# Kernel tuning notes

Measured on AMD Instinct MI355X. Metric: run time of the kernel, lower is better.

## Reference

```python
import jax, jax.numpy as jnp
import numpy as np

N, CIN, OUT, G, K = 16, 128, 128, 8, 56
GP = OUT // G  # group_planes = 16
EPS = 1e-5


def _bn(x, gamma, beta, mean, var, caxis):
    # inference-mode batchnorm over channel axis `caxis`
    shape = [1] * x.ndim
    shape[caxis] = x.shape[caxis]
    g = gamma.reshape(shape)
    b = beta.reshape(shape)
    m = mean.reshape(shape)
    v = var.reshape(shape)
    return (x - m) * (g * jax.lax.rsqrt(v + EPS)) + b


def setup_inputs() -> dict:
    key = jax.random.key(0)
    ks = jax.random.split(key, 16)
    d = {}
    d['x'] = jax.random.normal(ks[0], (N, CIN, K, K), jnp.float32)
    d['w_qkv'] = jax.random.normal(ks[1], (2 * OUT, CIN), jnp.float32) * np.float32(np.sqrt(1.0 / CIN))
    d['relative'] = jax.random.normal(ks[2], (2 * GP, 2 * K - 1), jnp.float32) * np.float32(np.sqrt(1.0 / GP))

    def bn_params(k, c):
        k1, k2, k3, k4 = jax.random.split(k, 4)
        gamma = 1.0 + 0.1 * jax.random.normal(k1, (c,), jnp.float32)
        beta = 0.05 * jax.random.normal(k2, (c,), jnp.float32)
        mean = 0.05 * jax.random.normal(k3, (c,), jnp.float32)
        var = 1.0 + 0.1 * jax.random.uniform(k4, (c,), jnp.float32)
        return gamma, beta, mean, var

    d['qkv_gamma'], d['qkv_beta'], d['qkv_mean'], d['qkv_var'] = bn_params(ks[3], 2 * OUT)
    d['sim_gamma'], d['sim_beta'], d['sim_mean'], d['sim_var'] = bn_params(ks[4], 3 * G)
    d['out_gamma'], d['out_beta'], d['out_mean'], d['out_var'] = bn_params(ks[5], 2 * OUT)
    return d


def reference(x, w_qkv, relative,
              qkv_gamma, qkv_beta, qkv_mean, qkv_var,
              sim_gamma, sim_beta, sim_mean, sim_var,
              out_gamma, out_beta, out_mean, out_var):
    n, c, h, w = x.shape  # width=False: attend along H
    xb = jnp.transpose(x, (0, 3, 1, 2)).reshape(n * w, c, h)  # [B, C, H], B = N*W

    # 1x1 conv qkv + BN1d
    qkv = jnp.einsum('oc,bch->boh', w_qkv, xb)  # [B, 2*OUT, H]
    qkv = _bn(qkv, qkv_gamma, qkv_beta, qkv_mean, qkv_var, 1)
    qkv = qkv.reshape(n * w, G, 2 * GP, h)
    hp = GP // 2
    q, k, v = qkv[:, :, :hp], qkv[:, :, hp:2 * hp], qkv[:, :, 2 * hp:]

    # relative position embeddings
    qi = jnp.arange(K)[None, :]
    ki = jnp.arange(K)[:, None]
    flat_idx = (ki - qi + K - 1).reshape(-1)  # [K*K]
    all_emb = relative[:, flat_idx].reshape(2 * GP, K, K)
    q_emb, k_emb, v_emb = all_emb[:hp], all_emb[hp:2 * hp], all_emb[2 * hp:]

    qr = jnp.einsum('bgci,cij->bgij', q, q_emb)
    kr = jnp.einsum('bgci,cij->bgij', k, k_emb).transpose(0, 1, 3, 2)
    qk = jnp.einsum('bgci,bgcj->bgij', q, k)

    stacked = jnp.concatenate([qk, qr, kr], axis=1)  # [B, 3G, H, H]
    stacked = _bn(stacked, sim_gamma, sim_beta, sim_mean, sim_var, 1)
    sim = stacked.reshape(n * w, 3, G, h, h).sum(axis=1)  # [B, G, H, H]
    sim = jax.nn.softmax(sim, axis=3)

    sv = jnp.einsum('bgij,bgcj->bgci', sim, v)      # [B, G, GP, H]
    sve = jnp.einsum('bgij,cij->bgci', sim, v_emb)  # [B, G, GP, H]
    # torch cat(dim=-1) then view(B, 2*OUT, H) == stack on a new axis before H
    stacked_out = jnp.concatenate([sv[:, :, :, None, :], sve[:, :, :, None, :]], axis=3)
    stacked_out = stacked_out.reshape(n * w, 2 * OUT, h)
    out = _bn(stacked_out, out_gamma, out_beta, out_mean, out_var, 1)
    out = out.reshape(n, w, OUT, 2, h).sum(axis=3)  # [N, W, OUT, H]
    out = jnp.transpose(out, (0, 2, 3, 1))  # [N, OUT, H, W]
    return out
```

## Files before the change

### kernel.cpp

```cpp
#include <hip/hip_runtime.h>
#include <hip/hip_bf16.h>
#include <cstddef>

#define EPSV 1e-5f

typedef __attribute__((ext_vector_type(8))) short bf16x8;
typedef __attribute__((ext_vector_type(4))) float f32x4;
typedef __attribute__((ext_vector_type(4))) short short4v;
typedef __attribute__((ext_vector_type(4))) int int4v;

__device__ __forceinline__ float b2f(short s) {
  union { unsigned u; float f; } x;
  x.u = ((unsigned)(unsigned short)s) << 16;
  return x.f;
}
__device__ __forceinline__ short f2b(float f) {
  union { __hip_bfloat16 h; short s; } x;
  x.h = __float2bfloat16(f);
  return x.s;
}

#define PF_W    3300000
#define PF_RQ   3316384
#define PF_RK   3327136
#define PF_RV   3337888
#define PF_QSC  3346592
#define PF_QSH  3346848
#define PF_OSC  3347104
#define PF_OSH  3347360
#define PF_SH3  3347616

__global__ __launch_bounds__(256) void k_prep(
    const float* __restrict__ wq, const float* __restrict__ rel,
    const float* __restrict__ qg, const float* __restrict__ qb,
    const float* __restrict__ qm, const float* __restrict__ qv,
    const float* __restrict__ sg, const float* __restrict__ sb,
    const float* __restrict__ sm, const float* __restrict__ svar,
    const float* __restrict__ og, const float* __restrict__ ob,
    const float* __restrict__ om, const float* __restrict__ ov,
    float* __restrict__ prep) {
  const int g = blockIdx.x;
  const int tid = threadIdx.x;
  const float scA = sg[g] * rsqrtf(svar[g] + EPSV);
  const float scB = sg[8 + g] * rsqrtf(svar[8 + g] + EPSV);
  const float scC = sg[16 + g] * rsqrtf(svar[16 + g] + EPSV);
  const float rCA = scC / scA;

  short* wb = (short*)(prep + PF_W) + g * 4096;
  for (int t = tid; t < 1024; t += 256) {
    int o = t >> 5, c0 = (t & 31) * 4;
    float4 wv = *(const float4*)&wq[g * 4096 + o * 128 + c0];
    short4v s4 = {f2b(wv.x), f2b(wv.y), f2b(wv.z), f2b(wv.w)};
    *(short4v*)&wb[o * 128 + c0] = s4;
  }
  float* rq = prep + PF_RQ + g * 1344;
  float* rk = prep + PF_RK + g * 1344;
  for (int t = tid; t < 1344; t += 256) {
    int d = t / 12, c = t - d * 12;
    rq[t] = (c < 8 && d < 111) ? rel[c * 111 + d] * scB : 0.f;
    rk[t] = (c < 8 && d < 111) ? rel[(8 + c) * 111 + d] * rCA : 0.f;
  }
  short* rv = (short*)(prep + PF_RV) + g * 2176;
  for (int t = tid; t < 2176; t += 256) {
    int c = t / 136, d = t - c * 136;
    rv[t] = (d < 111) ? f2b(rel[(16 + c) * 111 + d]) : (short)0;
  }
  if (tid < 32) {
    int ch = g * 32 + tid;
    float sc = qg[ch] * rsqrtf(qv[ch] + EPSV);
    float sh = qb[ch] - qm[ch] * sc;
    if (tid >= 8 && tid < 16) { sc *= scA; sh *= scA; }
    prep[PF_QSC + ch] = sc;
    prep[PF_QSH + ch] = sh;
    float so = og[ch] * rsqrtf(ov[ch] + EPSV);
    prep[PF_OSC + ch] = so;
    prep[PF_OSH + ch] = ob[ch] - om[ch] * so;
  }
  if (tid == 0) {
    float shA = sb[g] - sm[g] * scA;
    float shB = sb[8 + g] - sm[8 + g] * scB;
    float shC = sb[16 + g] - sm[16 + g] * scC;
    prep[PF_SH3 + g] = shA + shB + shC;
  }
}

__global__ __launch_bounds__(256) void k_transpose_in(const float* __restrict__ x,
                                                      unsigned* __restrict__ xbT) {
  const int nh = blockIdx.x;
  const int n = nh / 56, h = nh - n * 56;
  __shared__ short t2[128 * 57];
  const float* src = x + (size_t)n * 401408 + h * 56;
  for (int t = threadIdx.x; t < 1792; t += 256) {
    int c = t / 14, w4 = (t - c * 14) * 4;
    float4 v = *(const float4*)&src[c * 3136 + w4];
    t2[c * 57 + w4 + 0] = f2b(v.x);
    t2[c * 57 + w4 + 1] = f2b(v.y);
    t2[c * 57 + w4 + 2] = f2b(v.z);
    t2[c * 57 + w4 + 3] = f2b(v.w);
  }
  __syncthreads();
  for (int t = threadIdx.x; t < 3584; t += 256) {
    int w = t >> 6, cp = t & 63;
    unsigned lo = (unsigned short)t2[(2 * cp) * 57 + w];
    unsigned hi = (unsigned short)t2[(2 * cp + 1) * 57 + w];
    xbT[(((size_t)(n * 56 + w) * 56 + h) << 6) + cp] = lo | (hi << 16);
  }
}

__global__ __launch_bounds__(256) void k_transpose_out(const float* __restrict__ tmp,
                                                       float* __restrict__ out) {
  int nc = blockIdx.x;
  int n = nc >> 7, c = nc & 127;
  __shared__ float t[56][57];
  for (int idx = threadIdx.x; idx < 3136; idx += 256) {
    int w = idx / 56, h = idx - w * 56;
    t[h][w] = tmp[((size_t)(n * 56 + w) * 128 + c) * 56 + h];
  }
  __syncthreads();
  float* dst = out + (size_t)nc * 3136;
  for (int idx = threadIdx.x; idx < 3136; idx += 256)
    dst[idx] = t[idx / 56][idx % 56];
}

#define O_XST    0
#define O_SHFT   0
#define O_WS     7680
#define O_SIMA   7680
#define O_QKT    12288
#define O_SVL    12288
#define O_RQTF   14528
#define O_RKTF   17216
#define O_RELV   19904
#define O_VBH    22080
#define O_VBL    23232
#define SB_SH    24384

__global__ __launch_bounds__(512) void k_fused(
    const short* __restrict__ xbT, const float* __restrict__ prep,
    float* __restrict__ tmp) {
  const int tid = threadIdx.x;
  const int g = blockIdx.x / 896;
  const int b = blockIdx.x - g * 896;

  __shared__ __align__(16) short SB[SB_SH];
  __shared__ float s_qsc[32], s_qsh[32], s_osc[32], s_osh[32], s_sh3;

  const int lane = tid & 63;
  const int w = tid >> 6;
  const int m = lane & 15;
  const int qd = lane >> 4;
  const int it = w >> 1;
  const int half = w & 1;
  const int grp = tid >> 4;
  const int l16 = tid & 15;

  {
    int4v z = {0, 0, 0, 0};
    int4v* zp = (int4v*)(SB + O_VBH);
    for (int i = tid; i < 288; i += 512) zp[i] = z;

    const short* xsrc = xbT + (size_t)b * 7168;
    for (int t = tid; t < 896; t += 512) {
      int h = t >> 4, ck = (t & 15) * 8;
      *(bf16x8*)&SB[O_XST + h * 136 + ck] = *(const bf16x8*)&xsrc[h * 128 + ck];
    }
    const short* wsrc = (const short*)(prep + PF_W) + g * 4096;
    for (int t = tid; t < 512; t += 512) {
      int o = t >> 4, ck = (t & 15) * 8;
      *(bf16x8*)&SB[O_WS + o * 136 + ck] = *(const bf16x8*)&wsrc[o * 128 + ck];
    }
    const f32x4* rqp = (const f32x4*)(prep + PF_RQ + g * 1344);
    const f32x4* rkp = (const f32x4*)(prep + PF_RK + g * 1344);
    f32x4* rqd = (f32x4*)(SB + O_RQTF);
    f32x4* rkd = (f32x4*)(SB + O_RKTF);
    for (int t = tid; t < 672; t += 512) {
      if (t < 336) rqd[t] = rqp[t];
      else         rkd[t - 336] = rkp[t - 336];
    }
    const int4v* rvp = (const int4v*)((const short*)(prep + PF_RV) + g * 2176);
    int4v* rvd = (int4v*)(SB + O_RELV);
    for (int t = tid; t < 272; t += 512) rvd[t] = rvp[t];
    if (tid < 32) {
      s_qsc[tid] = prep[PF_QSC + g * 32 + tid];
      s_qsh[tid] = prep[PF_QSH + g * 32 + tid];
      s_osc[tid] = prep[PF_OSC + g * 32 + tid];
      s_osh[tid] = prep[PF_OSH + g * 32 + tid];
    }
    if (tid == 0) s_sh3 = prep[PF_SH3 + g];
  }
  __syncthreads();

  {
    const int o = half * 16 + m;
    const int h = it * 16 + m;
    f32x4 acc = {0.f, 0.f, 0.f, 0.f};
#pragma unroll
    for (int ks = 0; ks < 4; ++ks) {
      bf16x8 av = *(bf16x8*)&SB[O_WS + o * 136 + qd * 8 + ks * 32];
      bf16x8 bv = *(bf16x8*)&SB[O_XST + h * 136 + qd * 8 + ks * 32];
      acc = __builtin_amdgcn_mfma_f32_16x16x32_bf16(av, bv, acc, 0, 0, 0);
    }
    if (h < 56) {
      float* qkTf = (float*)(SB + O_QKT);
      if (half == 0) {
        float4 o4;
        o4.x = fmaf(acc[0], s_qsc[qd * 4 + 0], s_qsh[qd * 4 + 0]);
        o4.y = fmaf(acc[1], s_qsc[qd * 4 + 1], s_qsh[qd * 4 + 1]);
        o4.z = fmaf(acc[2], s_qsc[qd * 4 + 2], s_qsh[qd * 4 + 2]);
        o4.w = fmaf(acc[3], s_qsc[qd * 4 + 3], s_qsh[qd * 4 + 3]);
        *(float4*)&qkTf[h * 20 + qd * 4] = o4;
      } else {
#pragma unroll
        for (int r = 0; r < 4; ++r) {
          int cv = qd * 4 + r;
          float val = fmaf(acc[r], s_qsc[16 + cv], s_qsh[16 + cv]);
          short vh = f2b(val);
          short vl = f2b(val - b2f(vh));
          SB[O_VBH + cv * 72 + h] = vh;
          SB[O_VBL + cv * 72 + h] = vl;
        }
      }
    }
  }
  __syncthreads();

  {
    const float* qkTf = (const float*)(SB + O_QKT);
    const float* rqf = (const float*)(SB + O_RQTF);
    const float* rkf = (const float*)(SB + O_RKTF);
    const float sh3 = s_sh3;
    const int4v z = {0, 0, 0, 0};

    float4 kv0[4], kv1[4];
#pragma unroll
    for (int jt = 0; jt < 4; ++jt) {
      int j = jt * 16 + l16;
      int jj = (j < 56) ? j : 0;
      kv0[jt] = *(const float4*)&qkTf[jj * 20 + 8];
      kv1[jt] = *(const float4*)&qkTf[jj * 20 + 12];
    }

#pragma unroll
    for (int pass = 0; pass < 2; ++pass) {
      int i = pass * 32 + grp;
      if (i < 64 && l16 < 15) *(int4v*)&SB[O_SHFT + i * 120 + l16 * 8] = z;
      if (i < 56) {
        float4 qa = *(const float4*)&qkTf[i * 20 + 0];
        float4 qb4 = *(const float4*)&qkTf[i * 20 + 4];
        float L[4];
#pragma unroll
        for (int jt = 0; jt < 4; ++jt) {
          int j = jt * 16 + l16;
          if (j < 56) {
            const float4 rq0 = *(const float4*)&rqf[(i - j + 55) * 12];
            const float4 rq1 = *(const float4*)&rqf[(i - j + 55) * 12 + 4];
            const float4 rk0 = *(const float4*)&rkf[(j - i + 55) * 12];
            const float4 rk1 = *(const float4*)&rkf[(j - i + 55) * 12 + 4];
            const float4 k0 = kv0[jt], k1 = kv1[jt];
            float acc = sh3;
            acc = fmaf(qa.x, k0.x, acc);  acc = fmaf(qa.y, k0.y, acc);
            acc = fmaf(qa.z, k0.z, acc);  acc = fmaf(qa.w, k0.w, acc);
            acc = fmaf(qb4.x, k1.x, acc); acc = fmaf(qb4.y, k1.y, acc);
            acc = fmaf(qb4.z, k1.z, acc); acc = fmaf(qb4.w, k1.w, acc);
            acc = fmaf(qa.x, rq0.x, acc);  acc = fmaf(qa.y, rq0.y, acc);
            acc = fmaf(qa.z, rq0.z, acc);  acc = fmaf(qa.w, rq0.w, acc);
            acc = fmaf(qb4.x, rq1.x, acc); acc = fmaf(qb4.y, rq1.y, acc);
            acc = fmaf(qb4.z, rq1.z, acc); acc = fmaf(qb4.w, rq1.w, acc);
            acc = fmaf(k0.x, rk0.x, acc);  acc = fmaf(k0.y, rk0.y, acc);
            acc = fmaf(k0.z, rk0.z, acc);  acc = fmaf(k0.w, rk0.w, acc);
            acc = fmaf(k1.x, rk1.x, acc);  acc = fmaf(k1.y, rk1.y, acc);
            acc = fmaf(k1.w, rk1.w, acc);  acc = fmaf(k1.z, rk1.z, acc);
            L[jt] = acc;
          } else {
            L[jt] = -3.0e38f;
          }
        }
        float mx = fmaxf(fmaxf(L[0], L[1]), fmaxf(L[2], L[3]));
#pragma unroll
        for (int off = 1; off < 16; off <<= 1) mx = fmaxf(mx, __shfl_xor(mx, off));
        float sum = 0.f, ex[4];
#pragma unroll
        for (int jt = 0; jt < 4; ++jt) {
          ex[jt] = __expf(L[jt] - mx);
          sum += ex[jt];
        }
#pragma unroll
        for (int off = 1; off < 16; off <<= 1) sum += __shfl_xor(sum, off);
        float inv = 1.0f / sum;
#pragma unroll
        for (int jt = 0; jt < 4; ++jt) {
          int j = jt * 16 + l16;
          if (j < 56) {
            short pv = f2b(ex[jt] * inv);
            SB[O_SIMA + i * 72 + j] = pv;
            SB[O_SHFT + i * 120 + (i - j + 55)] = pv;
          } else {
            SB[O_SIMA + i * 72 + j] = 0;
          }
        }
      }
    }
  }
  __syncthreads();

  f32x4 sveacc = {0.f, 0.f, 0.f, 0.f};
  {
    if (half == 0) {
      bf16x8 pa0 = *(bf16x8*)&SB[O_SIMA + (it * 16 + m) * 72 + qd * 8];
      bf16x8 pa1 = *(bf16x8*)&SB[O_SIMA + (it * 16 + m) * 72 + qd * 8 + 32];
      f32x4 acc = {0.f, 0.f, 0.f, 0.f};
      bf16x8 bv;
      bv = *(bf16x8*)&SB[O_VBH + m * 72 + qd * 8];
      acc = __builtin_amdgcn_mfma_f32_16x16x32_bf16(pa0, bv, acc, 0, 0, 0);
      bv = *(bf16x8*)&SB[O_VBH + m * 72 + qd * 8 + 32];
      acc = __builtin_amdgcn_mfma_f32_16x16x32_bf16(pa1, bv, acc, 0, 0, 0);
      bv = *(bf16x8*)&SB[O_VBL + m * 72 + qd * 8];
      acc = __builtin_amdgcn_mfma_f32_16x16x32_bf16(pa0, bv, acc, 0, 0, 0);
      bv = *(bf16x8*)&SB[O_VBL + m * 72 + qd * 8 + 32];
      acc = __builtin_amdgcn_mfma_f32_16x16x32_bf16(pa1, bv, acc, 0, 0, 0);
      float* svLf = (float*)(SB + O_SVL);
#pragma unroll
      for (int r = 0; r < 4; ++r) {
        int i2 = it * 16 + qd * 4 + r;
        if (i2 < 56) svLf[m * 60 + i2] = acc[r];
      }
    } else {
#pragma unroll
      for (int ks = 0; ks < 4; ++ks) {
        bf16x8 av = *(bf16x8*)&SB[O_RELV + m * 136 + qd * 8 + ks * 32];
        bf16x8 bv = *(bf16x8*)&SB[O_SHFT + (it * 16 + m) * 120 + qd * 8 + ks * 32];
        sveacc = __builtin_amdgcn_mfma_f32_16x16x32_bf16(av, bv, sveacc, 0, 0, 0);
      }
    }
  }
  __syncthreads();

  if (half == 1) {
    const int i2 = it * 16 + m;
    if (i2 < 56) {
      const float* svLf = (const float*)(SB + O_SVL);
#pragma unroll
      for (int r = 0; r < 4; ++r) {
        int c = qd * 4 + r;
        float svv = svLf[c * 60 + i2];
        float o = fmaf(svv, s_osc[2 * c], s_osh[2 * c]) +
                  fmaf(sveacc[r], s_osc[2 * c + 1], s_osh[2 * c + 1]);
        tmp[((size_t)b * 128 + g * 16 + c) * 56 + i2] = o;
      }
    }
  }
}

extern "C" void kernel_launch(void* const* d_in, const int* in_sizes, int n_in,
                              void* d_out, int out_size, void* d_ws, size_t ws_size,
                              hipStream_t stream) {
  const float* x   = (const float*)d_in[0];
  const float* wq  = (const float*)d_in[1];
  const float* rel = (const float*)d_in[2];
  const float* qg = (const float*)d_in[3];
  const float* qb = (const float*)d_in[4];
  const float* qm = (const float*)d_in[5];
  const float* qv = (const float*)d_in[6];
  const float* sg = (const float*)d_in[7];
  const float* sb = (const float*)d_in[8];
  const float* sm = (const float*)d_in[9];
  const float* sv = (const float*)d_in[10];
  const float* og = (const float*)d_in[11];
  const float* ob = (const float*)d_in[12];
  const float* om = (const float*)d_in[13];
  const float* ov = (const float*)d_in[14];
  float* out = (float*)d_out;

  float* tmp = (float*)d_ws;

  k_prep<<<8, 256, 0, stream>>>(wq, rel, qg, qb, qm, qv,
                                sg, sb, sm, sv, og, ob, om, ov, out);
  k_transpose_in<<<896, 256, 0, stream>>>(x, (unsigned*)out);
  k_fused<<<7168, 512, 0, stream>>>((const short*)out, out, tmp);
  k_transpose_out<<<2048, 256, 0, stream>>>(tmp, out);
}
```

Baseline: 115.0 us.

## Merge prep and input transpose kernels, store intermediate in bf16, add MFMA priority

```diff
diff --git a/kernel.cpp b/kernel.cpp
--- a/kernel.cpp
+++ b/kernel.cpp
@@ -30,8 +30,9 @@
 #define PF_OSH  3347360
 #define PF_SH3  3347616
 
-__global__ __launch_bounds__(256) void k_prep(
-    const float* __restrict__ wq, const float* __restrict__ rel,
+__global__ __launch_bounds__(256) void k_prep_tin(
+    const float* __restrict__ x, const float* __restrict__ wq,
+    const float* __restrict__ rel,
     const float* __restrict__ qg, const float* __restrict__ qb,
     const float* __restrict__ qm, const float* __restrict__ qv,
     const float* __restrict__ sg, const float* __restrict__ sb,
@@ -39,82 +40,83 @@
     const float* __restrict__ og, const float* __restrict__ ob,
     const float* __restrict__ om, const float* __restrict__ ov,
     float* __restrict__ prep) {
-  const int g = blockIdx.x;
+  __shared__ short t2[128 * 57];
   const int tid = threadIdx.x;
-  const float scA = sg[g] * rsqrtf(svar[g] + EPSV);
-  const float scB = sg[8 + g] * rsqrtf(svar[8 + g] + EPSV);
-  const float scC = sg[16 + g] * rsqrtf(svar[16 + g] + EPSV);
-  const float rCA = scC / scA;
-
-  short* wb = (short*)(prep + PF_W) + g * 4096;
-  for (int t = tid; t < 1024; t += 256) {
-    int o = t >> 5, c0 = (t & 31) * 4;
-    float4 wv = *(const float4*)&wq[g * 4096 + o * 128 + c0];
-    short4v s4 = {f2b(wv.x), f2b(wv.y), f2b(wv.z), f2b(wv.w)};
-    *(short4v*)&wb[o * 128 + c0] = s4;
-  }
-  float* rq = prep + PF_RQ + g * 1344;
-  float* rk = prep + PF_RK + g * 1344;
-  for (int t = tid; t < 1344; t += 256) {
-    int d = t / 12, c = t - d * 12;
-    rq[t] = (c < 8 && d < 111) ? rel[c * 111 + d] * scB : 0.f;
-    rk[t] = (c < 8 && d < 111) ? rel[(8 + c) * 111 + d] * rCA : 0.f;
-  }
-  short* rv = (short*)(prep + PF_RV) + g * 2176;
-  for (int t = tid; t < 2176; t += 256) {
-    int c = t / 136, d = t - c * 136;
-    rv[t] = (d < 111) ? f2b(rel[(16 + c) * 111 + d]) : (short)0;
-  }
-  if (tid < 32) {
-    int ch = g * 32 + tid;
-    float sc = qg[ch] * rsqrtf(qv[ch] + EPSV);
-    float sh = qb[ch] - qm[ch] * sc;
-    if (tid >= 8 && tid < 16) { sc *= scA; sh *= scA; }
-    prep[PF_QSC + ch] = sc;
-    prep[PF_QSH + ch] = sh;
-    float so = og[ch] * rsqrtf(ov[ch] + EPSV);
-    prep[PF_OSC + ch] = so;
-    prep[PF_OSH + ch] = ob[ch] - om[ch] * so;
-  }
-  if (tid == 0) {
-    float shA = sb[g] - sm[g] * scA;
-    float shB = sb[8 + g] - sm[8 + g] * scB;
-    float shC = sb[16 + g] - sm[16 + g] * scC;
-    prep[PF_SH3 + g] = shA + shB + shC;
-  }
-}
-
-__global__ __launch_bounds__(256) void k_transpose_in(const float* __restrict__ x,
-                                                      unsigned* __restrict__ xbT) {
-  const int nh = blockIdx.x;
-  const int n = nh / 56, h = nh - n * 56;
-  __shared__ short t2[128 * 57];
-  const float* src = x + (size_t)n * 401408 + h * 56;
-  for (int t = threadIdx.x; t < 1792; t += 256) {
-    int c = t / 14, w4 = (t - c * 14) * 4;
-    float4 v = *(const float4*)&src[c * 3136 + w4];
-    t2[c * 57 + w4 + 0] = f2b(v.x);
-    t2[c * 57 + w4 + 1] = f2b(v.y);
-    t2[c * 57 + w4 + 2] = f2b(v.z);
-    t2[c * 57 + w4 + 3] = f2b(v.w);
-  }
-  __syncthreads();
-  for (int t = threadIdx.x; t < 3584; t += 256) {
-    int w = t >> 6, cp = t & 63;
-    unsigned lo = (unsigned short)t2[(2 * cp) * 57 + w];
-    unsigned hi = (unsigned short)t2[(2 * cp + 1) * 57 + w];
-    xbT[(((size_t)(n * 56 + w) * 56 + h) << 6) + cp] = lo | (hi << 16);
-  }
-}
-
-__global__ __launch_bounds__(256) void k_transpose_out(const float* __restrict__ tmp,
+
+  if (blockIdx.x < 8) {
+    const int g = blockIdx.x;
+    const float scA = sg[g] * rsqrtf(svar[g] + EPSV);
+    const float scB = sg[8 + g] * rsqrtf(svar[8 + g] + EPSV);
+    const float scC = sg[16 + g] * rsqrtf(svar[16 + g] + EPSV);
+    const float rCA = scC / scA;
+
+    short* wb = (short*)(prep + PF_W) + g * 4096;
+    for (int t = tid; t < 1024; t += 256) {
+      int o = t >> 5, c0 = (t & 31) * 4;
+      float4 wv = *(const float4*)&wq[g * 4096 + o * 128 + c0];
+      short4v s4 = {f2b(wv.x), f2b(wv.y), f2b(wv.z), f2b(wv.w)};
+      *(short4v*)&wb[o * 128 + c0] = s4;
+    }
+    float* rq = prep + PF_RQ + g * 1344;
+    float* rk = prep + PF_RK + g * 1344;
+    for (int t = tid; t < 1344; t += 256) {
+      int d = t / 12, c = t - d * 12;
+      rq[t] = (c < 8 && d < 111) ? rel[c * 111 + d] * scB : 0.f;
+      rk[t] = (c < 8 && d < 111) ? rel[(8 + c) * 111 + d] * rCA : 0.f;
+    }
+    short* rv = (short*)(prep + PF_RV) + g * 2176;
+    for (int t = tid; t < 2176; t += 256) {
+      int c = t / 136, d = t - c * 136;
+      rv[t] = (d < 111) ? f2b(rel[(16 + c) * 111 + d]) : (short)0;
+    }
+    if (tid < 32) {
+      int ch = g * 32 + tid;
+      float sc = qg[ch] * rsqrtf(qv[ch] + EPSV);
+      float sh = qb[ch] - qm[ch] * sc;
+      if (tid >= 8 && tid < 16) { sc *= scA; sh *= scA; }
+      prep[PF_QSC + ch] = sc;
+      prep[PF_QSH + ch] = sh;
+      float so = og[ch] * rsqrtf(ov[ch] + EPSV);
+      prep[PF_OSC + ch] = so;
+      prep[PF_OSH + ch] = ob[ch] - om[ch] * so;
+    }
+    if (tid == 0) {
+      float shA = sb[g] - sm[g] * scA;
+      float shB = sb[8 + g] - sm[8 + g] * scB;
+      float shC = sb[16 + g] - sm[16 + g] * scC;
+      prep[PF_SH3 + g] = shA + shB + shC;
+    }
+  } else {
+    const int nh = blockIdx.x - 8;
+    const int n = nh / 56, h = nh - n * 56;
+    unsigned* xbT = (unsigned*)prep;
+    const float* src = x + (size_t)n * 401408 + h * 56;
+    for (int t = tid; t < 1792; t += 256) {
+      int c = t / 14, w4 = (t - c * 14) * 4;
+      float4 v = *(const float4*)&src[c * 3136 + w4];
+      t2[c * 57 + w4 + 0] = f2b(v.x);
+      t2[c * 57 + w4 + 1] = f2b(v.y);
+      t2[c * 57 + w4 + 2] = f2b(v.z);
+      t2[c * 57 + w4 + 3] = f2b(v.w);
+    }
+    __syncthreads();
+    for (int t = tid; t < 3584; t += 256) {
+      int w = t >> 6, cp = t & 63;
+      unsigned lo = (unsigned short)t2[(2 * cp) * 57 + w];
+      unsigned hi = (unsigned short)t2[(2 * cp + 1) * 57 + w];
+      xbT[(((size_t)(n * 56 + w) * 56 + h) << 6) + cp] = lo | (hi << 16);
+    }
+  }
+}
+
+__global__ __launch_bounds__(256) void k_transpose_out(const short* __restrict__ tmp,
                                                        float* __restrict__ out) {
   int nc = blockIdx.x;
   int n = nc >> 7, c = nc & 127;
   __shared__ float t[56][57];
   for (int idx = threadIdx.x; idx < 3136; idx += 256) {
     int w = idx / 56, h = idx - w * 56;
-    t[h][w] = tmp[((size_t)(n * 56 + w) * 128 + c) * 56 + h];
+    t[h][w] = b2f(tmp[((size_t)(n * 56 + w) * 128 + c) * 56 + h]);
   }
   __syncthreads();
   float* dst = out + (size_t)nc * 3136;
@@ -137,7 +139,7 @@
 
 __global__ __launch_bounds__(512) void k_fused(
     const short* __restrict__ xbT, const float* __restrict__ prep,
-    float* __restrict__ tmp) {
+    short* __restrict__ tmp) {
   const int tid = threadIdx.x;
   const int g = blockIdx.x / 896;
   const int b = blockIdx.x - g * 896;
@@ -194,12 +196,14 @@
     const int o = half * 16 + m;
     const int h = it * 16 + m;
     f32x4 acc = {0.f, 0.f, 0.f, 0.f};
+    __builtin_amdgcn_s_setprio(1);
 #pragma unroll
     for (int ks = 0; ks < 4; ++ks) {
       bf16x8 av = *(bf16x8*)&SB[O_WS + o * 136 + qd * 8 + ks * 32];
       bf16x8 bv = *(bf16x8*)&SB[O_XST + h * 136 + qd * 8 + ks * 32];
       acc = __builtin_amdgcn_mfma_f32_16x16x32_bf16(av, bv, acc, 0, 0, 0);
     }
+    __builtin_amdgcn_s_setprio(0);
     if (h < 56) {
       float* qkTf = (float*)(SB + O_QKT);
       if (half == 0) {
@@ -310,6 +314,7 @@
       bf16x8 pa1 = *(bf16x8*)&SB[O_SIMA + (it * 16 + m) * 72 + qd * 8 + 32];
       f32x4 acc = {0.f, 0.f, 0.f, 0.f};
       bf16x8 bv;
+      __builtin_amdgcn_s_setprio(1);
       bv = *(bf16x8*)&SB[O_VBH + m * 72 + qd * 8];
       acc = __builtin_amdgcn_mfma_f32_16x16x32_bf16(pa0, bv, acc, 0, 0, 0);
       bv = *(bf16x8*)&SB[O_VBH + m * 72 + qd * 8 + 32];
@@ -318,6 +323,7 @@
       acc = __builtin_amdgcn_mfma_f32_16x16x32_bf16(pa0, bv, acc, 0, 0, 0);
       bv = *(bf16x8*)&SB[O_VBL + m * 72 + qd * 8 + 32];
       acc = __builtin_amdgcn_mfma_f32_16x16x32_bf16(pa1, bv, acc, 0, 0, 0);
+      __builtin_amdgcn_s_setprio(0);
       float* svLf = (float*)(SB + O_SVL);
 #pragma unroll
       for (int r = 0; r < 4; ++r) {
@@ -325,12 +331,14 @@
         if (i2 < 56) svLf[m * 60 + i2] = acc[r];
       }
     } else {
+      __builtin_amdgcn_s_setprio(1);
 #pragma unroll
       for (int ks = 0; ks < 4; ++ks) {
         bf16x8 av = *(bf16x8*)&SB[O_RELV + m * 136 + qd * 8 + ks * 32];
         bf16x8 bv = *(bf16x8*)&SB[O_SHFT + (it * 16 + m) * 120 + qd * 8 + ks * 32];
         sveacc = __builtin_amdgcn_mfma_f32_16x16x32_bf16(av, bv, sveacc, 0, 0, 0);
       }
+      __builtin_amdgcn_s_setprio(0);
     }
   }
   __syncthreads();
@@ -345,7 +353,7 @@
         float svv = svLf[c * 60 + i2];
         float o = fmaf(svv, s_osc[2 * c], s_osh[2 * c]) +
                   fmaf(sveacc[r], s_osc[2 * c + 1], s_osh[2 * c + 1]);
-        tmp[((size_t)b * 128 + g * 16 + c) * 56 + i2] = o;
+        tmp[((size_t)b * 128 + g * 16 + c) * 56 + i2] = f2b(o);
       }
     }
   }
@@ -371,11 +379,10 @@
   const float* ov = (const float*)d_in[14];
   float* out = (float*)d_out;
 
-  float* tmp = (float*)d_ws;
-
-  k_prep<<<8, 256, 0, stream>>>(wq, rel, qg, qb, qm, qv,
-                                sg, sb, sm, sv, og, ob, om, ov, out);
-  k_transpose_in<<<896, 256, 0, stream>>>(x, (unsigned*)out);
+  short* tmp = (short*)d_ws;
+
+  k_prep_tin<<<904, 256, 0, stream>>>(x, wq, rel, qg, qb, qm, qv,
+                                      sg, sb, sm, sv, og, ob, om, ov, out);
   k_fused<<<7168, 512, 0, stream>>>((const short*)out, out, tmp);
   k_transpose_out<<<2048, 256, 0, stream>>>(tmp, out);
 }
```

Result: faster. 110.0 us (-4.4%).
